# Kernel tuning notes

Measured on AMD Instinct MI355X. Metric: run time of the kernel, lower is better.

## Reference

```python
import jax, jax.numpy as jnp
import numpy as np

B, T, D = 4, 4096, 1024
H, HD = 16, 64
EPS = 1e-6


def setup_inputs() -> dict:
    key = jax.random.key(0)
    ks = jax.random.split(key, 5)
    scale = 1.0 / np.sqrt(D)
    return {
        "x": jax.random.normal(ks[0], (B, T, D), dtype=jnp.float32),
        "Wq": jax.random.normal(ks[1], (D, H * HD), dtype=jnp.float32) * scale,
        "Wk": jax.random.normal(ks[2], (D, H * HD), dtype=jnp.float32) * scale,
        "Wv": jax.random.normal(ks[3], (D, H * HD), dtype=jnp.float32) * scale,
        "Wo": jax.random.normal(ks[4], (H * HD, D), dtype=jnp.float32) * scale,
    }


def _feature_map(x):
    # ELU + 1 feature map (always positive)
    return jax.nn.elu(x) + 1.0


def _causal_linear_attention(q, k, v, eps=EPS):
    # q,k,v: (B,H,T,Dk/Dv) -> scan over T with running state
    Dk = q.shape[-1]
    Dv = v.shape[-1]
    qT = jnp.moveaxis(q, 2, 0)  # (T,B,H,Dk)
    kT = jnp.moveaxis(k, 2, 0)
    vT = jnp.moveaxis(v, 2, 0)

    S0 = jnp.zeros((q.shape[0], q.shape[1], Dk, Dv), dtype=q.dtype)
    z0 = jnp.zeros((q.shape[0], q.shape[1], Dk), dtype=q.dtype)

    def step(carry, qkv_t):
        S, z = carry
        q_t, k_t, v_t = qkv_t
        S = S + jnp.einsum('bhd,bhe->bhde', k_t, v_t)
        z = z + k_t
        num = jnp.einsum('bhd,bhde->bhe', q_t, S)
        den = jnp.einsum('bhd,bhd->bh', q_t, z) + eps
        return (S, z), num / den[..., None]

    _, yT = jax.lax.scan(step, (S0, z0), (qT, kT, vT))  # yT: (T,B,H,Dv)
    return jnp.moveaxis(yT, 0, 2)  # (B,H,T,Dv)


def reference(x, Wq, Wk, Wv, Wo):
    b, t, _ = x.shape

    def proj(W):
        return (x @ W).reshape(b, t, H, HD).transpose(0, 2, 1, 3)  # (B,H,T,HD)

    q = _feature_map(proj(Wq))
    k = _feature_map(proj(Wk))
    v = proj(Wv)
    y = _causal_linear_attention(q, k, v)  # (B,H,T,HD)
    y = y.transpose(0, 2, 1, 3).reshape(b, t, H * HD)
    return y @ Wo
```

## Files before the change

### kernel.cpp

```cpp
#include <hip/hip_runtime.h>


typedef __bf16 bf16;
typedef __bf16 bf16x4 __attribute__((ext_vector_type(4)));
typedef __bf16 bf16x8 __attribute__((ext_vector_type(8)));
typedef float f32x4 __attribute__((ext_vector_type(4)));

#define EPS 1e-6f

#define BAR() asm volatile("s_barrier" ::: "memory")
#define VMCNT4() asm volatile("s_waitcnt vmcnt(4)" ::: "memory")
#define VMCNT0() asm volatile("s_waitcnt vmcnt(0)" ::: "memory")

__device__ __forceinline__ void gl_lds16(const void* g, void* l) {
  __builtin_amdgcn_global_load_lds(
      (__attribute__((address_space(1))) void*)g,
      (__attribute__((address_space(3))) void*)l, 16, 0, 0);
}

__device__ __forceinline__ float fmact(float v) {
  return v > 0.f ? v + 1.f : __expf(v);
}

__global__ __launch_bounds__(256) void prep(const float* __restrict__ x,
                                            const float* __restrict__ Wq,
                                            const float* __restrict__ Wk,
                                            const float* __restrict__ Wv,
                                            const float* __restrict__ Wo,
                                            bf16* __restrict__ XB,
                                            bf16* __restrict__ WT3,
                                            bf16* __restrict__ WOT) {
  const int bid = blockIdx.x;
  const int t = threadIdx.x;
  if (bid < 8192) {
    size_t base = ((size_t)bid * 256 + t) * 8;
    float4 v0 = *(const float4*)&x[base];
    float4 v1 = *(const float4*)&x[base + 4];
    bf16x8 o;
    o[0] = (bf16)v0.x; o[1] = (bf16)v0.y; o[2] = (bf16)v0.z; o[3] = (bf16)v0.w;
    o[4] = (bf16)v1.x; o[5] = (bf16)v1.y; o[6] = (bf16)v1.z; o[7] = (bf16)v1.w;
    *(bf16x8*)&XB[base] = o;
    return;
  }
  __shared__ float tile[64][65];
  const int wi = (bid - 8192) >> 8;
  const int local = (bid - 8192) & 255;
  const float* W = (wi == 0) ? Wq : (wi == 1) ? Wk : (wi == 2) ? Wv : Wo;
  bf16* WT = (wi == 3) ? WOT : WT3 + (size_t)wi * 1048576;
  const int k0 = (local & 15) * 64, n0 = (local >> 4) * 64;
  {
    const int r4 = t / 16, c4 = (t % 16) * 4;
#pragma unroll
    for (int rr = 0; rr < 4; ++rr) {
      int r = r4 + rr * 16;
      float4 v = *(const float4*)&W[(size_t)(k0 + r) * 1024 + n0 + c4];
      tile[r][c4] = v.x; tile[r][c4 + 1] = v.y;
      tile[r][c4 + 2] = v.z; tile[r][c4 + 3] = v.w;
    }
  }
  __syncthreads();
  const int nl = t / 4, kb = (t % 4) * 16;
  bf16x8 o0, o1;
#pragma unroll
  for (int j = 0; j < 8; ++j) {
    o0[j] = (bf16)tile[kb + j][nl];
    o1[j] = (bf16)tile[kb + 8 + j][nl];
  }
  *(bf16x8*)&WT[(size_t)(n0 + nl) * 1024 + k0 + kb] = o0;
  *(bf16x8*)&WT[(size_t)(n0 + nl) * 1024 + k0 + kb + 8] = o1;
}

template <int PROJ>
__global__ __launch_bounds__(512, 2) void gemm8(const bf16* __restrict__ A,
                                                const bf16* __restrict__ BT,
                                                bf16* __restrict__ Obf,
                                                float* __restrict__ Of,
                                                const int N, const int gy) {
  extern __shared__ bf16 lds[];
  const int t = threadIdx.x;
  const int w = t >> 6, l = t & 63;
  const int nwg = (int)gridDim.x, cpx = nwg >> 3;
  const int f = ((int)blockIdx.x & 7) * cpx + ((int)blockIdx.x >> 3);
  const int bx = f / gy, by = f - bx * gy;
  const int m0 = bx * 256, n0 = by * 256;
  const int wm = (w >> 2) * 128, wn = (w & 3) * 64;
  const int lr = l & 15, lg = l >> 4;
  const int aslc = (w >> 2) * 8192;
  const int bslc = 16384 + ((w & 3) >> 1) * 8192;
  const int brow = (w & 1) * 64;
  const int srow = t >> 3;
  const int scol = ((t & 7) ^ ((t >> 3) & 7)) * 8;

  f32x4 acc[8][4] = {};
  bf16x8 bv[8];

#define FRAG(c, slc, sr_, ks_)                                          \
  (*(const bf16x8*)&lds[(c) * 32768 + (slc) + (sr_) * 64 +              \
                        (((ks_) * 32 + lg * 8) ^ (((sr_) & 7) << 3))])

#define STG(dbuf, slc, rbase, PTR, kt)                                        \
  do {                                                                        \
    const bf16* _s = (PTR) + (size_t)((rbase) + srow) * 1024 + (kt) * 64 + scol; \
    bf16* _d = lds + (dbuf) * 32768 + (slc) + w * 512;                        \
    gl_lds16(_s, _d);                                                         \
    gl_lds16(_s + 65536, _d + 4096);                                          \
  } while (0)

#define PHASE(c, q, STAGE_STMT, VM)                                           \
  {                                                                           \
    bf16x8 av[4];                                                             \
    _Pragma("unroll") for (int mi = 0; mi < 2; ++mi)                          \
      _Pragma("unroll") for (int kk = 0; kk < 2; ++kk)                        \
        av[mi * 2 + kk] = FRAG(c, aslc, (q) * 32 + mi * 16 + lr, kk);         \
    if ((q) == 0) {                                                           \
      _Pragma("unroll") for (int n = 0; n < 4; ++n)                           \
        _Pragma("unroll") for (int kk = 0; kk < 2; ++kk)                      \
          bv[n * 2 + kk] = FRAG(c, bslc, brow + n * 16 + lr, kk);             \
    }                                                                         \
    STAGE_STMT;                                                               \
    if (VM) VMCNT4();                                                         \
    __builtin_amdgcn_s_setprio(1);                                            \
    _Pragma("unroll") for (int mi = 0; mi < 2; ++mi)                          \
      _Pragma("unroll") for (int n = 0; n < 4; ++n)                           \
        _Pragma("unroll") for (int kk = 0; kk < 2; ++kk)                      \
          acc[(q) * 2 + mi][n] = __builtin_amdgcn_mfma_f32_16x16x32_bf16(     \
              av[mi * 2 + kk], bv[n * 2 + kk], acc[(q) * 2 + mi][n], 0, 0, 0);\
    __builtin_amdgcn_s_setprio(0);                                            \
    BAR();                                                                    \
  }

  STG(0, 0, m0, A, 0);        STG(0, 8192, m0 + 128, A, 0);
  STG(0, 16384, n0, BT, 0);   STG(0, 24576, n0 + 128, BT, 0);
  STG(1, 16384, n0, BT, 1);   STG(1, 24576, n0 + 128, BT, 1);
  VMCNT4();
  BAR();

#pragma unroll 1
  for (int I = 0; I < 8; ++I) {
    const int t2 = 2 * I;
    const int k1 = t2 + 1;
    const int k2 = (t2 + 2 > 15) ? 15 : t2 + 2;
    const int k3 = (t2 + 3 > 15) ? 15 : t2 + 3;
    PHASE(0, 0, STG(1, 0, m0, A, k1), 0);
    PHASE(0, 1, STG(1, 8192, m0 + 128, A, k1), 0);
    PHASE(0, 2, STG(0, 16384, n0, BT, k2), 0);
    PHASE(0, 3, STG(0, 24576, n0 + 128, BT, k2), 1);
    PHASE(1, 0, STG(0, 0, m0, A, k2), 0);
    PHASE(1, 1, STG(0, 8192, m0 + 128, A, k2), 0);
    PHASE(1, 2, STG(1, 16384, n0, BT, k3), 0);
    PHASE(1, 3, STG(1, 24576, n0 + 128, BT, k3), 1);
  }
  VMCNT0();
#undef PHASE
#undef STG
#undef FRAG
#pragma unroll
  for (int m = 0; m < 8; ++m)
#pragma unroll
    for (int n = 0; n < 4; ++n)
#pragma unroll
      for (int r = 0; r < 4; ++r) {
        int row = m0 + wm + m * 16 + lg * 4 + r;
        int col = n0 + wn + n * 16 + lr;
        float v = acc[m][n][r];
        if (PROJ) {
          if (col < 2048) v = fmact(v);
          Obf[(size_t)row * N + col] = (bf16)v;
        } else {
          Of[(size_t)row * N + col] = v;
        }
      }
}

__global__ __launch_bounds__(256) void chunk_ktv(const bf16* __restrict__ QKV,
                                                 float* __restrict__ S_ws,
                                                 float* __restrict__ z_ws) {
  const int blk = blockIdx.x;
  const int bh = blk >> 5, c = blk & 31;
  const int b = bh >> 4, h = bh & 15;
  const size_t rowbase = (size_t)b * 4096 + (size_t)c * 128;
  __shared__ alignas(16) bf16 KT[64 * 136];
  __shared__ alignas(16) bf16 VT[64 * 136];
  __shared__ float zpart[4][64];
  const int t = threadIdx.x;
  {
    const int r = t >> 1, c0 = (t & 1) * 32;
    const bf16* kp = QKV + (rowbase + r) * 3072 + 1024 + h * 64 + c0;
    const bf16* vp = QKV + (rowbase + r) * 3072 + 2048 + h * 64 + c0;
    bf16x8 kv[4], vv[4];
#pragma unroll
    for (int q8 = 0; q8 < 4; ++q8) {
      kv[q8] = *(const bf16x8*)&kp[q8 * 8];
      vv[q8] = *(const bf16x8*)&vp[q8 * 8];
    }
#pragma unroll
    for (int q8 = 0; q8 < 4; ++q8)
#pragma unroll
      for (int j = 0; j < 8; ++j) {
        KT[(c0 + q8 * 8 + j) * 136 + r] = kv[q8][j];
        VT[(c0 + q8 * 8 + j) * 136 + r] = vv[q8][j];
      }
  }
  __syncthreads();
  {
    const int d = t & 63, part = t >> 6;
    float zs = 0.f;
#pragma unroll
    for (int tt = 0; tt < 32; ++tt) zs += (float)KT[d * 136 + part * 32 + tt];
    zpart[part][d] = zs;
  }
  __syncthreads();
  if (t < 64)
    z_ws[(size_t)blk * 64 + t] =
        zpart[0][t] + zpart[1][t] + zpart[2][t] + zpart[3][t];
  const int l = t & 63, w = t >> 6;
  const int lr = l & 15, lg = l >> 4, lk = lg * 8;
  f32x4 acc[4] = {};
#pragma unroll
  for (int ks = 0; ks < 4; ++ks) {
    const int k0 = ks * 32;
    bf16x8 a = *(const bf16x8*)&VT[(w * 16 + lr) * 136 + k0 + lk];
#pragma unroll
    for (int n = 0; n < 4; ++n) {
      bf16x8 bk = *(const bf16x8*)&KT[(n * 16 + lr) * 136 + k0 + lk];
      acc[n] = __builtin_amdgcn_mfma_f32_16x16x32_bf16(a, bk, acc[n], 0, 0, 0);
    }
  }
#pragma unroll
  for (int n = 0; n < 4; ++n)
#pragma unroll
    for (int r = 0; r < 4; ++r) {
      int e = w * 16 + lg * 4 + r;
      int d = n * 16 + lr;
      S_ws[((size_t)blk * 64 + e) * 64 + d] = acc[n][r];
    }
}

__global__ __launch_bounds__(256) void prefix_scan(const float* __restrict__ S_ws,
                                                   const float* __restrict__ z_ws,
                                                   bf16* __restrict__ STp,
                                                   float* __restrict__ zP) {
  const int bh = blockIdx.x >> 2, dq = blockIdx.x & 3;
  const int t = threadIdx.x;
  const int e = t >> 2, d0 = dq * 16 + (t & 3) * 4;
  float r0 = 0.f, r1 = 0.f, r2 = 0.f, r3 = 0.f, zr = 0.f;
  const bool doz = (dq == 0) && (t < 64);
  const size_t base = (size_t)bh * 32;
  float4 v = *(const float4*)&S_ws[base * 4096 + e * 64 + d0];
  float zv = doz ? z_ws[base * 64 + t] : 0.f;
  for (int c = 0; c < 32; ++c) {
    float4 vn = {0.f, 0.f, 0.f, 0.f};
    float zn = 0.f;
    if (c < 31) {
      vn = *(const float4*)&S_ws[(base + c + 1) * 4096 + e * 64 + d0];
      if (doz) zn = z_ws[(base + c + 1) * 64 + t];
    }
    const size_t cb = base + c;
    bf16x4 o;
    o[0] = (bf16)r0; o[1] = (bf16)r1; o[2] = (bf16)r2; o[3] = (bf16)r3;
    *(bf16x4*)&STp[cb * 4096 + e * 64 + d0] = o;
    if (doz) zP[cb * 64 + t] = zr;
    r0 += v.x; r1 += v.y; r2 += v.z; r3 += v.w;
    zr += zv;
    v = vn; zv = zn;
  }
}

__global__ __launch_bounds__(256) void chunk_attn(const bf16* __restrict__ QKV,
                                                  const bf16* __restrict__ STp,
                                                  const float* __restrict__ zP,
                                                  bf16* __restrict__ Y) {
  const int blk = blockIdx.x;
  const int bh = blk >> 5, c = blk & 31;
  const int b = bh >> 4, h = bh & 15;
  const size_t cb = (size_t)bh * 32 + c;
  const size_t rowbase = (size_t)b * 4096 + (size_t)c * 128;
  const bf16* Q = QKV + rowbase * 3072 + h * 64;
  const bf16* K = QKV + rowbase * 3072 + 1024 + h * 64;
  const bf16* V = QKV + rowbase * 3072 + 2048 + h * 64;
  __shared__ alignas(16) bf16 VT[64 * 136];
  __shared__ alignas(16) bf16 P[128 * 136];
  __shared__ float den[128];
  const int t = threadIdx.x;
  {
    const int r = t >> 1, c0 = (t & 1) * 32;
    const bf16* vp = V + (size_t)r * 3072 + c0;
    bf16x8 vv[4];
#pragma unroll
    for (int q8 = 0; q8 < 4; ++q8) vv[q8] = *(const bf16x8*)&vp[q8 * 8];
#pragma unroll
    for (int q8 = 0; q8 < 4; ++q8)
#pragma unroll
      for (int j = 0; j < 8; ++j) VT[(c0 + q8 * 8 + j) * 136 + r] = vv[q8][j];
  }
  const int l = t & 63, w = t >> 6;
  const int lr = l & 15, lg = l >> 4, lk = lg * 8;
  f32x4 acc[2][4] = {};
  f32x4 accs[2][8] = {};
#pragma unroll
  for (int kq = 0; kq < 2; ++kq) {
    const int k0 = kq * 32;
    bf16x8 am[2];
#pragma unroll
    for (int m = 0; m < 2; ++m)
      am[m] = *(const bf16x8*)&Q[(size_t)(w * 32 + m * 16 + lr) * 3072 + k0 + lk];
#pragma unroll
    for (int n = 0; n < 4; ++n) {
      bf16x8 bs = *(const bf16x8*)&STp[cb * 4096 + (size_t)(n * 16 + lr) * 64 + k0 + lk];
#pragma unroll
      for (int m = 0; m < 2; ++m)
        acc[m][n] = __builtin_amdgcn_mfma_f32_16x16x32_bf16(am[m], bs, acc[m][n], 0, 0, 0);
    }
#pragma unroll
    for (int n = 0; n < 8; ++n) {
      bf16x8 bk = *(const bf16x8*)&K[(size_t)(n * 16 + lr) * 3072 + k0 + lk];
#pragma unroll
      for (int m = 0; m < 2; ++m)
        accs[m][n] = __builtin_amdgcn_mfma_f32_16x16x32_bf16(am[m], bk, accs[m][n], 0, 0, 0);
    }
  }
#pragma unroll
  for (int m = 0; m < 2; ++m)
#pragma unroll
    for (int r = 0; r < 4; ++r) {
      const int row_c = w * 32 + m * 16 + lg * 4 + r;
      float s = 0.f;
#pragma unroll
      for (int n = 0; n < 8; ++n) {
        const int col_c = n * 16 + lr;
        float v = accs[m][n][r];
        v = (col_c <= row_c) ? v : 0.f;
        accs[m][n][r] = v;
        s += v;
      }
      s += __shfl_xor(s, 1);
      s += __shfl_xor(s, 2);
      s += __shfl_xor(s, 4);
      s += __shfl_xor(s, 8);
      if (lr == 0) den[row_c] = s;
#pragma unroll
      for (int n = 0; n < 8; ++n)
        P[row_c * 136 + n * 16 + lr] = (bf16)accs[m][n][r];
    }
  __syncthreads();
  if (t < 128) {
    float s = EPS;
    const bf16* qr = Q + (size_t)t * 3072;
    const float* zp = zP + cb * 64;
#pragma unroll
    for (int d8 = 0; d8 < 64; d8 += 8) {
      bf16x8 qv = *(const bf16x8*)&qr[d8];
#pragma unroll
      for (int j = 0; j < 8; ++j) s += (float)qv[j] * zp[d8 + j];
    }
    den[t] += s;
  }
#pragma unroll
  for (int ks = 0; ks < 4; ++ks) {
    const int k0 = ks * 32;
    bf16x8 ap[2];
#pragma unroll
    for (int m = 0; m < 2; ++m)
      ap[m] = *(const bf16x8*)&P[(w * 32 + m * 16 + lr) * 136 + k0 + lk];
#pragma unroll
    for (int n = 0; n < 4; ++n) {
      bf16x8 bv = *(const bf16x8*)&VT[(n * 16 + lr) * 136 + k0 + lk];
#pragma unroll
      for (int m = 0; m < 2; ++m)
        acc[m][n] = __builtin_amdgcn_mfma_f32_16x16x32_bf16(ap[m], bv, acc[m][n], 0, 0, 0);
    }
  }
  __syncthreads();
#pragma unroll
  for (int m = 0; m < 2; ++m)
#pragma unroll
    for (int n = 0; n < 4; ++n)
#pragma unroll
      for (int r = 0; r < 4; ++r) {
        const int row_c = w * 32 + m * 16 + lg * 4 + r;
        const int col = n * 16 + lr;
        float y = acc[m][n][r] / den[row_c];
        Y[(rowbase + row_c) * 1024 + h * 64 + col] = (bf16)y;
      }
}

extern "C" void kernel_launch(void* const* d_in, const int* in_sizes, int n_in,
                              void* d_out, int out_size, void* d_ws, size_t ws_size,
                              hipStream_t stream) {
  (void)in_sizes; (void)n_in; (void)out_size; (void)ws_size;
  const float* x  = (const float*)d_in[0];
  const float* Wq = (const float*)d_in[1];
  const float* Wk = (const float*)d_in[2];
  const float* Wv = (const float*)d_in[3];
  const float* Wo = (const float*)d_in[4];
  char* ws = (char*)d_ws;
  bf16*  XB   = (bf16*)ws;
  bf16*  WT3  = (bf16*)(ws + 33554432);
  bf16*  WOT  = (bf16*)(ws + 39845888);
  bf16*  QKV  = (bf16*)(ws + 41943040);
  float* S_ws = (float*)(ws + 142606336);
  float* z_ws = (float*)(ws + 176160768);
  bf16*  STp  = (bf16*)(ws + 176685056);
  float* zP   = (float*)(ws + 193462272);
  bf16*  Y    = XB;

  {
    auto k1 = gemm8<1>; auto k0 = gemm8<0>;
    (void)hipFuncSetAttribute((const void*)k1,
        hipFuncAttributeMaxDynamicSharedMemorySize, 131072);
    (void)hipFuncSetAttribute((const void*)k0,
        hipFuncAttributeMaxDynamicSharedMemorySize, 131072);
  }

  prep<<<9216, 256, 0, stream>>>(x, Wq, Wk, Wv, Wo, XB, WT3, WOT);
  gemm8<1><<<768, 512, 131072, stream>>>(XB, WT3, QKV, nullptr, 3072, 12);
  chunk_ktv<<<2048, 256, 0, stream>>>(QKV, S_ws, z_ws);
  prefix_scan<<<256, 256, 0, stream>>>(S_ws, z_ws, STp, zP);
  chunk_attn<<<2048, 256, 0, stream>>>(QKV, STp, zP, Y);
  gemm8<0><<<256, 512, 131072, stream>>>(Y, WOT, nullptr, (float*)d_out, 1024, 4);
}
```

Measured before the change: 263.7 us.

## Replace 256x256 GEMM tiles with 128x256 tiles and triple-buffered K=32 pipeline

Rewrites the bf16 MFMA GEMM used for the QKV and output projections. Block tiles shrink from 256x256 to 128x256 and the K step from 64 to 32. A three-stage LDS ring replaces the double buffer, and the launch bound is raised to allow more resident blocks. The intent is more blocks per GPU (1536 and 512 instead of 768 and 256) for better CU fill and latency hiding. In exchange, each block reuses operands less and pays more barriers per K step.

```diff
diff --git a/kernel.cpp b/kernel.cpp
--- a/kernel.cpp
+++ b/kernel.cpp
@@ -9,7 +9,7 @@
 #define EPS 1e-6f
 
 #define BAR() asm volatile("s_barrier" ::: "memory")
-#define VMCNT4() asm volatile("s_waitcnt vmcnt(4)" ::: "memory")
+#define VMCNT3() asm volatile("s_waitcnt vmcnt(3)" ::: "memory")
 #define VMCNT0() asm volatile("s_waitcnt vmcnt(0)" ::: "memory")
 
 __device__ __forceinline__ void gl_lds16(const void* g, void* l) {
@@ -71,7 +71,7 @@
 }
 
 template <int PROJ>
-__global__ __launch_bounds__(512, 2) void gemm8(const bf16* __restrict__ A,
+__global__ __launch_bounds__(512, 4) void gemm2(const bf16* __restrict__ A,
                                                 const bf16* __restrict__ BT,
                                                 bf16* __restrict__ Obf,
                                                 float* __restrict__ Of,
@@ -82,80 +82,70 @@
   const int nwg = (int)gridDim.x, cpx = nwg >> 3;
   const int f = ((int)blockIdx.x & 7) * cpx + ((int)blockIdx.x >> 3);
   const int bx = f / gy, by = f - bx * gy;
-  const int m0 = bx * 256, n0 = by * 256;
-  const int wm = (w >> 2) * 128, wn = (w & 3) * 64;
+  const int m0 = bx * 128, n0 = by * 256;
+  const int wm = (w >> 2) * 64, wn = (w & 3) * 64;
   const int lr = l & 15, lg = l >> 4;
-  const int aslc = (w >> 2) * 8192;
-  const int bslc = 16384 + ((w & 3) >> 1) * 8192;
-  const int brow = (w & 1) * 64;
-  const int srow = t >> 3;
-  const int scol = ((t & 7) ^ ((t >> 3) & 7)) * 8;
-
-  f32x4 acc[8][4] = {};
-  bf16x8 bv[8];
-
-#define FRAG(c, slc, sr_, ks_)                                          \
-  (*(const bf16x8*)&lds[(c) * 32768 + (slc) + (sr_) * 64 +              \
-                        (((ks_) * 32 + lg * 8) ^ (((sr_) & 7) << 3))])
-
-#define STG(dbuf, slc, rbase, PTR, kt)                                        \
+  const int srow = t >> 2;
+  const int scol = ((t & 3) ^ ((t >> 2) & 3)) * 8;
+  const bf16* pa  = A  + (size_t)(m0 + srow) * 1024 + scol;
+  const bf16* pb0 = BT + (size_t)(n0 + srow) * 1024 + scol;
+  const bf16* pb1 = BT + (size_t)(n0 + 128 + srow) * 1024 + scol;
+
+  f32x4 acc[4][4] = {};
+
+#define FRAGA(sb, sr_)                                                  \
+  (*(const bf16x8*)&lds[(sb) * 12288 + (sr_) * 32 +                     \
+                        (((lg) ^ ((sr_) & 3)) << 3)])
+#define FRAGB(sb, sr_)                                                  \
+  (*(const bf16x8*)&lds[(sb) * 12288 + 4096 + (sr_) * 32 +              \
+                        (((lg) ^ ((sr_) & 3)) << 3)])
+
+#define STG(sb, kt)                                                           \
   do {                                                                        \
-    const bf16* _s = (PTR) + (size_t)((rbase) + srow) * 1024 + (kt) * 64 + scol; \
-    bf16* _d = lds + (dbuf) * 32768 + (slc) + w * 512;                        \
-    gl_lds16(_s, _d);                                                         \
-    gl_lds16(_s + 65536, _d + 4096);                                          \
+    bf16* _da = lds + (sb) * 12288 + w * 512;                                 \
+    gl_lds16(pa + (kt) * 32, _da);                                            \
+    gl_lds16(pb0 + (kt) * 32, _da + 4096);                                    \
+    gl_lds16(pb1 + (kt) * 32, _da + 8192);                                    \
   } while (0)
 
-#define PHASE(c, q, STAGE_STMT, VM)                                           \
+#define TILE(cb, sb2, kt2)                                                    \
   {                                                                           \
-    bf16x8 av[4];                                                             \
-    _Pragma("unroll") for (int mi = 0; mi < 2; ++mi)                          \
-      _Pragma("unroll") for (int kk = 0; kk < 2; ++kk)                        \
-        av[mi * 2 + kk] = FRAG(c, aslc, (q) * 32 + mi * 16 + lr, kk);         \
-    if ((q) == 0) {                                                           \
+    bf16x8 av[4], bv[4];                                                      \
+    _Pragma("unroll") for (int m = 0; m < 4; ++m)                             \
+      av[m] = FRAGA(cb, wm + m * 16 + lr);                                    \
+    _Pragma("unroll") for (int n = 0; n < 4; ++n)                             \
+      bv[n] = FRAGB(cb, wn + n * 16 + lr);                                    \
+    STG(sb2, kt2);                                                            \
+    __builtin_amdgcn_s_setprio(1);                                            \
+    _Pragma("unroll") for (int m = 0; m < 4; ++m)                             \
       _Pragma("unroll") for (int n = 0; n < 4; ++n)                           \
-        _Pragma("unroll") for (int kk = 0; kk < 2; ++kk)                      \
-          bv[n * 2 + kk] = FRAG(c, bslc, brow + n * 16 + lr, kk);             \
-    }                                                                         \
-    STAGE_STMT;                                                               \
-    if (VM) VMCNT4();                                                         \
-    __builtin_amdgcn_s_setprio(1);                                            \
-    _Pragma("unroll") for (int mi = 0; mi < 2; ++mi)                          \
-      _Pragma("unroll") for (int n = 0; n < 4; ++n)                           \
-        _Pragma("unroll") for (int kk = 0; kk < 2; ++kk)                      \
-          acc[(q) * 2 + mi][n] = __builtin_amdgcn_mfma_f32_16x16x32_bf16(     \
-              av[mi * 2 + kk], bv[n * 2 + kk], acc[(q) * 2 + mi][n], 0, 0, 0);\
+        acc[m][n] = __builtin_amdgcn_mfma_f32_16x16x32_bf16(                  \
+            av[m], bv[n], acc[m][n], 0, 0, 0);                                \
     __builtin_amdgcn_s_setprio(0);                                            \
+    VMCNT3();                                                                 \
     BAR();                                                                    \
   }
 
-  STG(0, 0, m0, A, 0);        STG(0, 8192, m0 + 128, A, 0);
-  STG(0, 16384, n0, BT, 0);   STG(0, 24576, n0 + 128, BT, 0);
-  STG(1, 16384, n0, BT, 1);   STG(1, 24576, n0 + 128, BT, 1);
-  VMCNT4();
+  STG(0, 0);
+  STG(1, 1);
+  VMCNT3();
   BAR();
 
 #pragma unroll 1
-  for (int I = 0; I < 8; ++I) {
-    const int t2 = 2 * I;
-    const int k1 = t2 + 1;
-    const int k2 = (t2 + 2 > 15) ? 15 : t2 + 2;
-    const int k3 = (t2 + 3 > 15) ? 15 : t2 + 3;
-    PHASE(0, 0, STG(1, 0, m0, A, k1), 0);
-    PHASE(0, 1, STG(1, 8192, m0 + 128, A, k1), 0);
-    PHASE(0, 2, STG(0, 16384, n0, BT, k2), 0);
-    PHASE(0, 3, STG(0, 24576, n0 + 128, BT, k2), 1);
-    PHASE(1, 0, STG(0, 0, m0, A, k2), 0);
-    PHASE(1, 1, STG(0, 8192, m0 + 128, A, k2), 0);
-    PHASE(1, 2, STG(1, 16384, n0, BT, k3), 0);
-    PHASE(1, 3, STG(1, 24576, n0 + 128, BT, k3), 1);
-  }
+  for (int tt = 0; tt < 30; tt += 3) {
+    TILE(0, 2, tt + 2);
+    TILE(1, 0, tt + 3);
+    TILE(2, 1, tt + 4 > 31 ? 31 : tt + 4);
+  }
+  TILE(0, 2, 31);
+  TILE(1, 0, 31);
   VMCNT0();
-#undef PHASE
+#undef TILE
 #undef STG
-#undef FRAG
-#pragma unroll
-  for (int m = 0; m < 8; ++m)
+#undef FRAGB
+#undef FRAGA
+#pragma unroll
+  for (int m = 0; m < 4; ++m)
 #pragma unroll
     for (int n = 0; n < 4; ++n)
 #pragma unroll
@@ -405,17 +395,17 @@
   bf16*  Y    = XB;
 
   {
-    auto k1 = gemm8<1>; auto k0 = gemm8<0>;
+    auto k1 = gemm2<1>; auto k0 = gemm2<0>;
     (void)hipFuncSetAttribute((const void*)k1,
-        hipFuncAttributeMaxDynamicSharedMemorySize, 131072);
+        hipFuncAttributeMaxDynamicSharedMemorySize, 73728);
     (void)hipFuncSetAttribute((const void*)k0,
-        hipFuncAttributeMaxDynamicSharedMemorySize, 131072);
+        hipFuncAttributeMaxDynamicSharedMemorySize, 73728);
   }
 
   prep<<<9216, 256, 0, stream>>>(x, Wq, Wk, Wv, Wo, XB, WT3, WOT);
-  gemm8<1><<<768, 512, 131072, stream>>>(XB, WT3, QKV, nullptr, 3072, 12);
+  gemm2<1><<<1536, 512, 73728, stream>>>(XB, WT3, QKV, nullptr, 3072, 12);
   chunk_ktv<<<2048, 256, 0, stream>>>(QKV, S_ws, z_ws);
   prefix_scan<<<256, 256, 0, stream>>>(S_ws, z_ws, STp, zP);
   chunk_attn<<<2048, 256, 0, stream>>>(QKV, STp, zP, Y);
-  gemm8<0><<<256, 512, 131072, stream>>>(Y, WOT, nullptr, (float*)d_out, 1024, 4);
-}
+  gemm2<0><<<512, 512, 73728, stream>>>(Y, WOT, nullptr, (float*)d_out, 1024, 4);
+}
```

New measurement: 279.8 us, median of 3. 6.1% more time.
